# Kernel tuning notes

Measured on AMD Instinct MI355X. Metric: run time of the kernel, lower is better.

## Reference

```python
import jax, jax.numpy as jnp
import numpy as np

DIM = 128
B = 262144


def setup_inputs() -> dict:
    key = jax.random.key(0)
    k_t, k_w1, k_b1, k_w2, k_b2 = jax.random.split(key, 5)
    t = jax.random.uniform(k_t, (B,), dtype=jnp.float32)  # t in [0, 1]
    s = 1.0 / np.sqrt(DIM)  # torch Linear default init scale
    W1 = jax.random.uniform(k_w1, (DIM, DIM), dtype=jnp.float32, minval=-s, maxval=s)
    b1 = jax.random.uniform(k_b1, (DIM,), dtype=jnp.float32, minval=-s, maxval=s)
    W2 = jax.random.uniform(k_w2, (DIM, DIM), dtype=jnp.float32, minval=-s, maxval=s)
    b2 = jax.random.uniform(k_b2, (DIM,), dtype=jnp.float32, minval=-s, maxval=s)
    return {"t": t, "W1": W1, "b1": b1, "W2": W2, "b2": b2}


def reference(t, W1, b1, W2, b2):
    # create_timestep_embedding, vectorized over batch and dim:
    #   emb[b, i] = t[b]*cos(i/dim*pi*t[b]) + t[b]*sin(i/dim*pi*(1 - t[b]))
    phase = (jnp.arange(DIM, dtype=t.dtype) / DIM) * jnp.pi  # [DIM]
    tb = t[:, None]  # [B, 1]
    emb = tb * jnp.cos(phase[None, :] * tb) + tb * jnp.sin(phase[None, :] * (1.0 - tb))  # [B, DIM]
    x = jax.nn.silu(emb @ W1.T + b1)  # Linear128 + SiLU
    x = jax.nn.silu(x @ W2.T + b2)    # Linear128 + SiLU
    return x
```

## Files before the change

kernel.cpp:

```cpp
#include <hip/hip_runtime.h>

typedef _Float16 f16;
typedef _Float16 f16x2 __attribute__((ext_vector_type(2)));
typedef _Float16 f16x8 __attribute__((ext_vector_type(8)));
typedef float    f32x4 __attribute__((ext_vector_type(4)));

#define DIM 128

__device__ __forceinline__ float silu_f(float x) {
    float e = __builtin_amdgcn_exp2f(x * -1.44269504088896341f);
    return x * __builtin_amdgcn_rcpf(1.0f + e);
}

__global__ __launch_bounds__(256, 2)
void ts_mlp_kernel(const float* __restrict__ t,
                   const float* __restrict__ W1, const float* __restrict__ b1,
                   const float* __restrict__ W2, const float* __restrict__ b2,
                   float* __restrict__ out, int B) {
    __shared__ f16x8 w1f[4][8][64];
    __shared__ f16x8 w2f[4][8][64];
    __shared__ f16x2 x1p[4][256][4];

    const int tid  = threadIdx.x;
    const int wv   = tid >> 6;
    const int lane = tid & 63;
    const int q    = lane >> 4;
    const int ln   = lane & 15;
    const int par  = lane & 1;

    for (int mtx = 0; mtx < 2; ++mtx) {
        const float* W = mtx ? W2 : W1;
        for (int nti = 0; nti < 2; ++nti) {
            const int nt = wv * 2 + nti;
            const int n  = nt * 16 + ln;
            for (int kt = 0; kt < 4; ++kt) {
                const int k0 = kt * 32 + q * 8;
                const float4* src = (const float4*)(W + n * DIM + k0);
                float4 lo = src[0], hi = src[1];
                f16x8 fr;
                fr[0] = (f16)lo.x; fr[1] = (f16)lo.y; fr[2] = (f16)lo.z; fr[3] = (f16)lo.w;
                fr[4] = (f16)hi.x; fr[5] = (f16)hi.y; fr[6] = (f16)hi.z; fr[7] = (f16)hi.w;
                if (mtx) w2f[kt][nt][lane] = fr; else w1f[kt][nt][lane] = fr;
            }
        }
    }
    float b1v[8], b2v[8];
#pragma unroll
    for (int nt = 0; nt < 8; ++nt) {
        b1v[nt] = b1[nt * 16 + ln];
        b2v[nt] = b2[nt * 16 + ln];
    }
    __syncthreads();

    const int ntiles = B >> 6;
    for (int tile = blockIdx.x; tile < ntiles; tile += gridDim.x) {
        const int row0 = tile * 64 + wv * 16;

        const float tv   = t[row0 + ln];
        const float t256 = tv * 0.00390625f;
        const float o256 = (1.0f - tv) * 0.00390625f;
        f16x8 af[4];
#pragma unroll
        for (int kt = 0; kt < 4; ++kt) {
#pragma unroll
            for (int j = 0; j < 8; ++j) {
                const float fd = (float)(kt * 32 + q * 8 + j);
                const float c  = __builtin_amdgcn_cosf(fd * t256);
                const float s  = __builtin_amdgcn_sinf(fd * o256);
                af[kt][j] = (f16)(tv * (c + s));
            }
        }

        f32x4 acc[8];
#pragma unroll
        for (int nt = 0; nt < 8; ++nt) acc[nt] = (f32x4){0.f, 0.f, 0.f, 0.f};
#pragma unroll
        for (int kt = 0; kt < 4; ++kt) {
#pragma unroll
            for (int nt = 0; nt < 8; ++nt) {
                acc[nt] = __builtin_amdgcn_mfma_f32_16x16x32_f16(
                    af[kt], w1f[kt][nt][lane], acc[nt], 0, 0, 0);
            }
        }

#pragma unroll
        for (int nt = 0; nt < 8; ++nt) {
            float v[4], pv[4];
#pragma unroll
            for (int r = 0; r < 4; ++r) v[r] = silu_f(acc[nt][r] + b1v[nt]);
#pragma unroll
            for (int r = 0; r < 4; ++r) pv[r] = __shfl_xor(v[r], 1, 64);
            const int k0  = nt * 16 + (ln & 14);
            const int cch = k0 >> 3;
            const int hw  = (k0 & 7) >> 1;
#pragma unroll
            for (int p = 0; p < 2; ++p) {
                const int r = par * 2 + p;
                const int m = q * 4 + r;
                const float lo = par ? pv[r] : v[r];
                const float hi = par ? v[r] : pv[r];
                f16x2 h; h.x = (f16)lo; h.y = (f16)hi;
                x1p[wv][m * 16 + (cch ^ m)][hw] = h;
            }
        }

        f32x4 acc2[8];
#pragma unroll
        for (int nt = 0; nt < 8; ++nt) acc2[nt] = (f32x4){0.f, 0.f, 0.f, 0.f};
#pragma unroll
        for (int kt = 0; kt < 4; ++kt) {
            const f16x8 a2 = *(const f16x8*)&x1p[wv][ln * 16 + ((kt * 4 + q) ^ ln)][0];
#pragma unroll
            for (int nt = 0; nt < 8; ++nt) {
                acc2[nt] = __builtin_amdgcn_mfma_f32_16x16x32_f16(
                    a2, w2f[kt][nt][lane], acc2[nt], 0, 0, 0);
            }
        }

#pragma unroll
        for (int nt = 0; nt < 8; ++nt) {
#pragma unroll
            for (int r = 0; r < 4; ++r) {
                const float o = silu_f(acc2[nt][r] + b2v[nt]);
                out[(size_t)(row0 + q * 4 + r) * DIM + nt * 16 + ln] = o;
            }
        }
    }
}

extern "C" void kernel_launch(void* const* d_in, const int* in_sizes, int n_in,
                              void* d_out, int out_size, void* d_ws, size_t ws_size,
                              hipStream_t stream) {
    const float* t  = (const float*)d_in[0];
    const float* W1 = (const float*)d_in[1];
    const float* b1 = (const float*)d_in[2];
    const float* W2 = (const float*)d_in[3];
    const float* b2 = (const float*)d_in[4];
    float* out = (float*)d_out;
    const int B = in_sizes[0];
    const int ntiles = B >> 6;
    int grid = ntiles < 512 ? ntiles : 512;
    ts_mlp_kernel<<<dim3(grid), dim3(256), 0, stream>>>(t, W1, b1, W2, b2, out, B);
}
```

Measured before the change: 191.9 us.

## Keep weight fragments in registers and split output columns across waves

Each wave now holds fp16 fragments for its own 32 output columns of W1 and W2 in registers instead of staging both full matrices in LDS. The embedding tile and hidden activations are shared through LDS so every wave computes all 64 rows of the tile, with block-wide barriers between stages. The grid changes from a 512-block persistent loop to one block per four tiles (1024 blocks), and occupancy is raised to 3 blocks per SIMD. The intent is to cut LDS traffic and footprint, at the cost of re-reading and converting the weights in every block and adding three syncthreads per tile.

```diff
diff --git a/kernel.cpp b/kernel.cpp
--- a/kernel.cpp
+++ b/kernel.cpp
@@ -12,14 +12,13 @@
     return x * __builtin_amdgcn_rcpf(1.0f + e);
 }
 
-__global__ __launch_bounds__(256, 2)
+__global__ __launch_bounds__(256, 3)
 void ts_mlp_kernel(const float* __restrict__ t,
                    const float* __restrict__ W1, const float* __restrict__ b1,
                    const float* __restrict__ W2, const float* __restrict__ b2,
                    float* __restrict__ out, int B) {
-    __shared__ f16x8 w1f[4][8][64];
-    __shared__ f16x8 w2f[4][8][64];
-    __shared__ f16x2 x1p[4][256][4];
+    __shared__ f16x8 embf[4][4][64];
+    __shared__ f16x2 x1s[1024][4];
 
     const int tid  = threadIdx.x;
     const int wv   = tid >> 6;
@@ -28,103 +27,122 @@
     const int ln   = lane & 15;
     const int par  = lane & 1;
 
-    for (int mtx = 0; mtx < 2; ++mtx) {
-        const float* W = mtx ? W2 : W1;
-        for (int nti = 0; nti < 2; ++nti) {
-            const int nt = wv * 2 + nti;
-            const int n  = nt * 16 + ln;
-            for (int kt = 0; kt < 4; ++kt) {
-                const int k0 = kt * 32 + q * 8;
-                const float4* src = (const float4*)(W + n * DIM + k0);
-                float4 lo = src[0], hi = src[1];
-                f16x8 fr;
-                fr[0] = (f16)lo.x; fr[1] = (f16)lo.y; fr[2] = (f16)lo.z; fr[3] = (f16)lo.w;
-                fr[4] = (f16)hi.x; fr[5] = (f16)hi.y; fr[6] = (f16)hi.z; fr[7] = (f16)hi.w;
-                if (mtx) w2f[kt][nt][lane] = fr; else w1f[kt][nt][lane] = fr;
-            }
+    const int ntiles = B >> 6;
+
+    float t4[4];
+#pragma unroll
+    for (int ti = 0; ti < 4; ++ti) {
+        const int tile = blockIdx.x * 4 + ti;
+        t4[ti] = (tile < ntiles) ? t[tile * 64 + wv * 16 + ln] : 0.0f;
+    }
+
+    f16x8 w1f[4][2], w2f[4][2];
+    float b1v[2], b2v[2];
+#pragma unroll
+    for (int u = 0; u < 2; ++u) {
+        const int n = wv * 32 + u * 16 + ln;
+        b1v[u] = b1[n];
+        b2v[u] = b2[n];
+#pragma unroll
+        for (int kt = 0; kt < 4; ++kt) {
+            const float4* p1 = (const float4*)(W1 + n * DIM + kt * 32 + q * 8);
+            const float4* p2 = (const float4*)(W2 + n * DIM + kt * 32 + q * 8);
+            const float4 a = p1[0], b = p1[1], c = p2[0], d = p2[1];
+            f16x8 f1, f2;
+            f1[0]=(f16)a.x; f1[1]=(f16)a.y; f1[2]=(f16)a.z; f1[3]=(f16)a.w;
+            f1[4]=(f16)b.x; f1[5]=(f16)b.y; f1[6]=(f16)b.z; f1[7]=(f16)b.w;
+            f2[0]=(f16)c.x; f2[1]=(f16)c.y; f2[2]=(f16)c.z; f2[3]=(f16)c.w;
+            f2[4]=(f16)d.x; f2[5]=(f16)d.y; f2[6]=(f16)d.z; f2[7]=(f16)d.w;
+            w1f[kt][u] = f1;
+            w2f[kt][u] = f2;
         }
     }
-    float b1v[8], b2v[8];
-#pragma unroll
-    for (int nt = 0; nt < 8; ++nt) {
-        b1v[nt] = b1[nt * 16 + ln];
-        b2v[nt] = b2[nt * 16 + ln];
-    }
-    __syncthreads();
 
-    const int ntiles = B >> 6;
-    for (int tile = blockIdx.x; tile < ntiles; tile += gridDim.x) {
-        const int row0 = tile * 64 + wv * 16;
+#pragma unroll 1
+    for (int ti = 0; ti < 4; ++ti) {
+        const int tile = blockIdx.x * 4 + ti;
+        if (tile >= ntiles) break;
+        const int row0 = tile * 64;
 
-        const float tv   = t[row0 + ln];
+        const float tv   = t4[ti];
         const float t256 = tv * 0.00390625f;
         const float o256 = (1.0f - tv) * 0.00390625f;
-        f16x8 af[4];
+        const float qb   = (float)(q * 8);
 #pragma unroll
         for (int kt = 0; kt < 4; ++kt) {
+            f16x8 ef;
 #pragma unroll
             for (int j = 0; j < 8; ++j) {
-                const float fd = (float)(kt * 32 + q * 8 + j);
+                const float fd = (float)(kt * 32 + j) + qb;
                 const float c  = __builtin_amdgcn_cosf(fd * t256);
                 const float s  = __builtin_amdgcn_sinf(fd * o256);
-                af[kt][j] = (f16)(tv * (c + s));
+                ef[j] = (f16)(tv * (c + s));
             }
+            embf[wv][kt][lane] = ef;
         }
+        __syncthreads();
 
-        f32x4 acc[8];
+        f32x4 acc[4][2];
 #pragma unroll
-        for (int nt = 0; nt < 8; ++nt) acc[nt] = (f32x4){0.f, 0.f, 0.f, 0.f};
+        for (int mt = 0; mt < 4; ++mt) {
+            acc[mt][0] = (f32x4){0.f,0.f,0.f,0.f};
+            acc[mt][1] = (f32x4){0.f,0.f,0.f,0.f};
 #pragma unroll
-        for (int kt = 0; kt < 4; ++kt) {
-#pragma unroll
-            for (int nt = 0; nt < 8; ++nt) {
-                acc[nt] = __builtin_amdgcn_mfma_f32_16x16x32_f16(
-                    af[kt], w1f[kt][nt][lane], acc[nt], 0, 0, 0);
+            for (int kt = 0; kt < 4; ++kt) {
+                const f16x8 af = embf[mt][kt][lane];
+                acc[mt][0] = __builtin_amdgcn_mfma_f32_16x16x32_f16(af, w1f[kt][0], acc[mt][0], 0, 0, 0);
+                acc[mt][1] = __builtin_amdgcn_mfma_f32_16x16x32_f16(af, w1f[kt][1], acc[mt][1], 0, 0, 0);
             }
         }
 
 #pragma unroll
-        for (int nt = 0; nt < 8; ++nt) {
-            float v[4], pv[4];
+        for (int mt = 0; mt < 4; ++mt) {
 #pragma unroll
-            for (int r = 0; r < 4; ++r) v[r] = silu_f(acc[nt][r] + b1v[nt]);
+            for (int u = 0; u < 2; ++u) {
+                float v[4], pv[4];
 #pragma unroll
-            for (int r = 0; r < 4; ++r) pv[r] = __shfl_xor(v[r], 1, 64);
-            const int k0  = nt * 16 + (ln & 14);
-            const int cch = k0 >> 3;
-            const int hw  = (k0 & 7) >> 1;
+                for (int r = 0; r < 4; ++r) v[r] = silu_f(acc[mt][u][r] + b1v[u]);
 #pragma unroll
-            for (int p = 0; p < 2; ++p) {
-                const int r = par * 2 + p;
-                const int m = q * 4 + r;
-                const float lo = par ? pv[r] : v[r];
-                const float hi = par ? v[r] : pv[r];
-                f16x2 h; h.x = (f16)lo; h.y = (f16)hi;
-                x1p[wv][m * 16 + (cch ^ m)][hw] = h;
+                for (int r = 0; r < 4; ++r) pv[r] = __shfl_xor(v[r], 1, 64);
+                const int k0  = wv * 32 + u * 16 + (ln & 14);
+                const int cch = k0 >> 3;
+                const int hw  = (k0 & 7) >> 1;
+#pragma unroll
+                for (int p = 0; p < 2; ++p) {
+                    const int r = par * 2 + p;
+                    const int m = mt * 16 + q * 4 + r;
+                    const float lo = par ? pv[r] : v[r];
+                    const float hi = par ? v[r] : pv[r];
+                    f16x2 h; h.x = (f16)lo; h.y = (f16)hi;
+                    x1s[m * 16 + (cch ^ (m & 15))][hw] = h;
+                }
             }
         }
+        __syncthreads();
 
-        f32x4 acc2[8];
 #pragma unroll
-        for (int nt = 0; nt < 8; ++nt) acc2[nt] = (f32x4){0.f, 0.f, 0.f, 0.f};
+        for (int mt = 0; mt < 4; ++mt) {
+            f32x4 a2c[2];
+            a2c[0] = (f32x4){0.f,0.f,0.f,0.f};
+            a2c[1] = (f32x4){0.f,0.f,0.f,0.f};
 #pragma unroll
-        for (int kt = 0; kt < 4; ++kt) {
-            const f16x8 a2 = *(const f16x8*)&x1p[wv][ln * 16 + ((kt * 4 + q) ^ ln)][0];
+            for (int kt = 0; kt < 4; ++kt) {
+                const int m = mt * 16 + ln;
+                const f16x8 a2 = *(const f16x8*)&x1s[m * 16 + ((kt * 4 + q) ^ ln)][0];
+                a2c[0] = __builtin_amdgcn_mfma_f32_16x16x32_f16(a2, w2f[kt][0], a2c[0], 0, 0, 0);
+                a2c[1] = __builtin_amdgcn_mfma_f32_16x16x32_f16(a2, w2f[kt][1], a2c[1], 0, 0, 0);
+            }
 #pragma unroll
-            for (int nt = 0; nt < 8; ++nt) {
-                acc2[nt] = __builtin_amdgcn_mfma_f32_16x16x32_f16(
-                    a2, w2f[kt][nt][lane], acc2[nt], 0, 0, 0);
+            for (int u = 0; u < 2; ++u) {
+                const int col = wv * 32 + u * 16 + ln;
+                const size_t rbase = (size_t)(row0 + mt * 16 + q * 4) * DIM + col;
+#pragma unroll
+                for (int r = 0; r < 4; ++r) {
+                    out[rbase + (size_t)r * DIM] = silu_f(a2c[u][r] + b2v[u]);
+                }
             }
         }
-
-#pragma unroll
-        for (int nt = 0; nt < 8; ++nt) {
-#pragma unroll
-            for (int r = 0; r < 4; ++r) {
-                const float o = silu_f(acc2[nt][r] + b2v[nt]);
-                out[(size_t)(row0 + q * 4 + r) * DIM + nt * 16 + ln] = o;
-            }
-        }
+        __syncthreads();
     }
 }
 
@@ -139,6 +157,6 @@
     float* out = (float*)d_out;
     const int B = in_sizes[0];
     const int ntiles = B >> 6;
-    int grid = ntiles < 512 ? ntiles : 512;
+    const int grid = (ntiles + 3) >> 2;
     ts_mlp_kernel<<<dim3(grid), dim3(256), 0, stream>>>(t, W1, b1, W2, b2, out, B);
 }
```

After: 221.6 us. 1.15x slower.
